# Kernel tuning notes

Measured on AMD Instinct MI355X. Metric: run time of the kernel, lower is better.

Reference implementation:

```python
import jax, jax.numpy as jnp
import numpy as np
from jax.ops import segment_sum, segment_max

N, E, B = 100000, 400000, 2048
F_NODE, F_EDGE, G_DIM = 7, 3, 10
HID, H, C, L, T = 128, 4, 32, 4, 5
EPS = 1e-5
NEG_SLOPE = 0.2

def setup_inputs():
    key = jax.random.key(0)
    ks = iter(jax.random.split(key, 64))
    def nrm(shape, fan_in):
        return jax.random.normal(next(ks), shape, jnp.float32) / np.float32(np.sqrt(fan_in))
    return {
        "x": jax.random.normal(next(ks), (N, F_NODE), jnp.float32),
        "edge_index": jax.random.randint(next(ks), (2, E), 0, N),
        "edge_attr": jax.random.normal(next(ks), (E, F_EDGE), jnp.float32),
        "batch": jnp.sort(jax.random.randint(next(ks), (N,), 0, B)),
        "global_features": jax.random.normal(next(ks), (B, G_DIM), jnp.float32),
        "node_w": nrm((F_NODE, HID), F_NODE), "node_b": jnp.zeros((HID,), jnp.float32),
        "edge_w": nrm((F_EDGE, HID), F_EDGE), "edge_b": jnp.zeros((HID,), jnp.float32),
        "gat_lin_w": nrm((L, HID, H * C), HID),
        "gat_edge_w": nrm((L, HID, H * C), HID),
        "att_src": nrm((L, H, C), C), "att_dst": nrm((L, H, C), C), "att_edge": nrm((L, H, C), C),
        "gat_bias": jnp.zeros((L, H * C), jnp.float32),
        "bn_gamma": jnp.ones((L, HID), jnp.float32), "bn_beta": jnp.zeros((L, HID), jnp.float32),
        "bn_mean": jnp.zeros((L, HID), jnp.float32), "bn_var": jnp.ones((L, HID), jnp.float32),
        "gc_w": nrm((3 * HID, HID), 3 * HID), "gc_b": jnp.zeros((HID,), jnp.float32),
        "gf1_w": nrm((G_DIM, HID // 2), G_DIM), "gf1_b": jnp.zeros((HID // 2,), jnp.float32),
        "gf2_w": nrm((HID // 2, HID // 2), HID // 2), "gf2_b": jnp.zeros((HID // 2,), jnp.float32),
        "p1_w": nrm((HID + HID // 2, HID), HID + HID // 2), "p1_b": jnp.zeros((HID,), jnp.float32),
        "p2_w": nrm((HID, HID // 2), HID), "p2_b": jnp.zeros((HID // 2,), jnp.float32),
        "p3_w": nrm((HID // 2, T), HID // 2), "p3_b": jnp.zeros((T,), jnp.float32),
    }

def _forward(x, edge_attr, global_features,
             node_w, node_b, edge_w, edge_b,
             gat_lin_w, gat_edge_w, att_src, att_dst, att_edge, gat_bias,
             bn_gamma, bn_beta, bn_mean, bn_var,
             gc_w, gc_b, gf1_w, gf1_b, gf2_w, gf2_b,
             p1_w, p1_b, p2_w, p2_b, p3_w, p3_b,
             edge_index, batch):
    n = x.shape[0]
    b = global_features.shape[0]
    src, dst = edge_index[0], edge_index[1]
    loop = jnp.arange(n)

    h = x @ node_w + node_b                       # [N, HID]
    e = edge_attr @ edge_w + edge_b               # [E, HID]

    # PyG add_self_loops with fill_value='mean': self-loop edge feature is the
    # mean of incoming edge features (0 for isolated nodes).
    deg = segment_sum(jnp.ones((src.shape[0],), h.dtype), dst, num_segments=n)
    e_loop = segment_sum(e, dst, num_segments=n) / jnp.maximum(deg, 1.0)[:, None]
    fsrc = jnp.concatenate([src, loop])
    fdst = jnp.concatenate([dst, loop])
    fe = jnp.concatenate([e, e_loop], axis=0)     # [E+N, HID]

    for i in range(L):
        h_res = h
        xh = (h @ gat_lin_w[i]).reshape(n, H, C)
        eh = (fe @ gat_edge_w[i]).reshape(-1, H, C)
        a_s = jnp.einsum('nhc,hc->nh', xh, att_src[i])
        a_d = jnp.einsum('nhc,hc->nh', xh, att_dst[i])
        a_e = jnp.einsum('ehc,hc->eh', eh, att_edge[i])
        alpha = jax.nn.leaky_relu(a_s[fsrc] + a_d[fdst] + a_e, NEG_SLOPE)  # [E+N, H]
        # segment softmax over destination neighborhoods (self loops => nonempty)
        amax = segment_max(alpha, fdst, num_segments=n)
        expa = jnp.exp(alpha - amax[fdst])
        denom = segment_sum(expa, fdst, num_segments=n)
        coef = expa / denom[fdst]
        out = segment_sum(xh[fsrc] * coef[..., None], fdst, num_segments=n)
        out = out.reshape(n, H * C) + gat_bias[i]
        # BatchNorm (eval-mode running stats)
        out = (out - bn_mean[i]) * (bn_gamma[i] / jnp.sqrt(bn_var[i] + EPS)) + bn_beta[i]
        h = jax.nn.relu(out) + h_res

    # multi-pool readout
    cnt = segment_sum(jnp.ones((n,), h.dtype), batch, num_segments=b)
    gsum = segment_sum(h, batch, num_segments=b)
    gmean = gsum / jnp.maximum(cnt, 1.0)[:, None]
    gmax = segment_max(h, batch, num_segments=b)
    gmax = jnp.where(cnt[:, None] > 0, gmax, 0.0)
    graph = jnp.concatenate([gmean, gmax, gsum], axis=1)   # [B, 3*HID]
    graph = jax.nn.relu(graph @ gc_w + gc_b)
    glob = jax.nn.relu(global_features @ gf1_w + gf1_b) @ gf2_w + gf2_b
    comb = jnp.concatenate([graph, glob], axis=1)          # [B, HID + HID//2]
    hid = jax.nn.relu(comb @ p1_w + p1_b)
    hid = jax.nn.relu(hid @ p2_w + p2_b)
    return hid @ p3_w + p3_b                               # [B, T]

def reference(x, edge_index, edge_attr, batch, global_features,
              node_w, node_b, edge_w, edge_b,
              gat_lin_w, gat_edge_w, att_src, att_dst, att_edge, gat_bias,
              bn_gamma, bn_beta, bn_mean, bn_var,
              gc_w, gc_b, gf1_w, gf1_b, gf2_w, gf2_b,
              p1_w, p1_b, p2_w, p2_b, p3_w, p3_b):
    return _forward(x, edge_attr, global_features,
                    node_w, node_b, edge_w, edge_b,
                    gat_lin_w, gat_edge_w, att_src, att_dst, att_edge, gat_bias,
                    bn_gamma, bn_beta, bn_mean, bn_var,
                    gc_w, gc_b, gf1_w, gf1_b, gf2_w, gf2_b,
                    p1_w, p1_b, p2_w, p2_b, p3_w, p3_b,
                    edge_index, batch)
```

## Files before the change

kernel.cpp:

```cpp
#include <hip/hip_runtime.h>

#define N_NODES 100000
#define N_EDGES 400000
#define N_GRAPHS 2048
#define HID 128
#define NLAYER 4
#define TOUT 5
#define EPSV 1e-5f
#define SLOPE 0.2f
#define MAXDEG 32
#define NB 98

typedef float v4f __attribute__((ext_vector_type(4)));
typedef __bf16 v8bf __attribute__((ext_vector_type(8)));

static __device__ __forceinline__ unsigned short f2bf_bits(float f){
  unsigned u = __builtin_bit_cast(unsigned, f);
  unsigned r = u + 0x7fffu + ((u >> 16) & 1u);
  return (unsigned short)(r >> 16);
}
static __device__ __forceinline__ float bfbits2f(unsigned short s){
  unsigned u = ((unsigned)s) << 16;
  return __builtin_bit_cast(float, u);
}
static __device__ __forceinline__ float bflo(unsigned u){
  return __builtin_bit_cast(float, u << 16);
}
static __device__ __forceinline__ float bfhi(unsigned u){
  return __builtin_bit_cast(float, u & 0xffff0000u);
}
static __device__ __forceinline__ float lrelu(float v){
  return v>0.f ? v : SLOPE*v;
}


__global__ void k_setup(const float* __restrict__ gat_edge_w, const float* __restrict__ att_edge,
                        const float* __restrict__ edge_w, const float* __restrict__ edge_b,
                        const float* __restrict__ gat_bias, const float* __restrict__ gamma,
                        const float* __restrict__ beta, const float* __restrict__ mean,
                        const float* __restrict__ var, const float* __restrict__ gat_lin_w,
                        const float* __restrict__ att_src, const float* __restrict__ att_dst,
                        float* __restrict__ mebuf, float* __restrict__ bnA, float* __restrict__ bnS,
                        unsigned short* __restrict__ whiE, unsigned short* __restrict__ wloE,
                        unsigned short* __restrict__ whi,
                        int* __restrict__ deg, int* __restrict__ fill){
  __shared__ float Ve[128*16];
  int bid = blockIdx.x, t = threadIdx.x;
  if(bid == 0){
    for(int i=t; i<NLAYER*HID; i+=256){
      int l_ = i>>7, pos = i&127, lane = pos>>2, j = pos&3;
      int ch = ((lane>>3)<<5) + ((lane&7)<<1) + ((j&1)<<4) + (j>>1);
      int src = l_*128 + ch;
      float A = gamma[src]*rsqrtf(var[src]+EPSV);
      bnA[i] = A;
      bnS[i] = (gat_bias[src]-mean[src])*A + beta[src];
    }
    for(int id=t; id<2048; id+=256){
      int k = id>>4, li = id&15, l = li>>2, hh = li&3;
      const float* gw = gat_edge_w + l*16384 + k*128 + hh*32;
      const float* at = att_edge + l*128 + hh*32;
      float s = 0.f;
      #pragma unroll
      for(int c=0;c<32;++c) s += gw[c]*at[c];
      Ve[k*16+li] = s;
    }
    __syncthreads();
    if(t < 48){
      int f = t>>4, li = t&15;
      float s=0.f;
      for(int k=0;k<128;++k) s += edge_w[f*128+k]*Ve[k*16+li];
      mebuf[f*16+li] = s;
    } else if (t < 64){
      int li = t-48; float s=0.f;
      for(int k=0;k<128;++k) s += edge_b[k]*Ve[k*16+li];
      mebuf[48+li] = s;
    }
  } else if(bid <= 1024){
    int wave = t>>6, lane = t&63;
    int i = (bid-1)*8 + wave*2 + (lane>>5);
    int l_ = i>>11, rest = i&2047, kp = rest>>4, col = rest&15;
    int sub = lane&31;
    float val = 0.f;
    if(col < 8){
      int h_ = col&3, isdst = col>>2;
      int ch = ((kp>>5)<<5) + ((kp&1)<<4) + ((kp&31)>>1);
      const float* at = (isdst? att_dst : att_src);
      val = gat_lin_w[l_*16384 + ch*128 + h_*32 + sub] * at[l_*128 + h_*32 + sub];
    }
    val += __shfl_xor(val,1); val += __shfl_xor(val,2); val += __shfl_xor(val,4);
    val += __shfl_xor(val,8); val += __shfl_xor(val,16);
    if(sub == 0){
      unsigned short hi = f2bf_bits(val);
      unsigned short lo = f2bf_bits(val - bfbits2f(hi));
      int kb=kp>>5, quad=(kp>>3)&3, jj=kp&7, lane2=quad*16+col;
      int dst = ((l_*4+kb)*64 + lane2)*8 + jj;
      whiE[dst]=hi; wloE[dst]=lo;
    }
  } else if(bid <= 1280){
    int tg = (bid-1025)*256 + t;
    int base = tg>>9, off = tg&511;
    int l = base>>5, kb=(base>>3)&3, cg=base&7;
    int lane = off>>3, j = off&7;
    int quad = lane>>4, r = lane&15;
    int kp = kb*32 + quad*8 + j;
    int k = ((kp>>5)<<5) | ((kp&1)<<4) | ((kp&31)>>1);
    whi[tg] = f2bf_bits(gat_lin_w[l*16384 + k*128 + cg*16 + r]);
  } else {
    int tg = (bid-1281)*256 + t;
    if(tg < N_NODES){ deg[tg]=0; fill[tg]=0; }
  }
}

__global__ void k_init(const float* __restrict__ x, const float* __restrict__ nw,
                       const float* __restrict__ nb, unsigned* __restrict__ h16,
                       const int* __restrict__ ei, int* __restrict__ deg){
  int bid = blockIdx.x, t = threadIdx.x;
  if(bid < N_NODES/4){
    int node = bid*4 + (t>>6);
    int c = t&63;
    int ch = ((c>>4)<<5) + (c&15);
    float a0 = nb[ch], a1 = nb[ch+16];
    #pragma unroll
    for(int f=0; f<7; ++f){
      float xv = x[node*7+f];
      a0 += xv*nw[f*HID+ch];
      a1 += xv*nw[f*HID+ch+16];
    }
    unsigned p = (unsigned)f2bf_bits(a0) | ((unsigned)f2bf_bits(a1)<<16);
    h16[(size_t)node*64 + c] = p;
  } else {
    int e = (bid - N_NODES/4)*256 + t;
    if(e < N_EDGES) atomicAdd(&deg[ei[N_EDGES+e]], 1);
  }
}

__global__ void k_scan1(const int* __restrict__ deg, int* __restrict__ part){
  __shared__ int s[256];
  int t=threadIdx.x; int base = blockIdx.x*1024 + t*4;
  int sum=0;
  #pragma unroll
  for(int j=0;j<4;++j){ int i=base+j; sum += (i<N_NODES)? deg[i]:0; }
  s[t]=sum; __syncthreads();
  for(int off=128; off>0; off>>=1){ if(t<off) s[t]+=s[t+off]; __syncthreads(); }
  if(t==0) part[blockIdx.x]=s[0];
}
__global__ void k_scan3(const int* __restrict__ deg, const int* __restrict__ part,
                        int* __restrict__ rowptr){
  __shared__ int s[256];
  int t=threadIdx.x, b=blockIdx.x;
  int g = 0, tot = 0;
  for(int i=0;i<NB;++i){ int v = part[i]; g += (i<b)? v : 0; tot += v; }
  if(b==0 && t==0) rowptr[N_NODES]=tot;
  int base = b*1024 + t*4;
  int v[4]; int sum=0; int pre[4];
  #pragma unroll
  for(int j=0;j<4;++j){ int i=base+j; v[j]=(i<N_NODES)?deg[i]:0; pre[j]=sum; sum+=v[j]; }
  s[t]=sum; __syncthreads();
  for(int off=1; off<256; off<<=1){
    int xv = (t>=off)? s[t-off]:0; __syncthreads();
    s[t]+=xv; __syncthreads();
  }
  int toff = (t>0)? s[t-1]:0;
  #pragma unroll
  for(int j=0;j<4;++j){ int i=base+j; if(i<N_NODES) rowptr[i]=g+toff+pre[j]; }
}

__global__ void k_fill(const int* __restrict__ ei, const float* __restrict__ ea,
                       const int* __restrict__ rowptr, int* __restrict__ fill,
                       int* __restrict__ csr_src, float* __restrict__ ea_csr){
  int e = blockIdx.x*256+threadIdx.x;
  if(e>=N_EDGES) return;
  int dst = ei[N_EDGES+e];
  int pos = rowptr[dst] + atomicAdd(&fill[dst],1);
  csr_src[pos] = ei[e];
  v4f q = {ea[e*3], ea[e*3+1], ea[e*3+2], 0.f};
  ((v4f*)ea_csr)[pos] = q;
}

__global__ void k_gemm(const unsigned short* __restrict__ h16,
                       const unsigned short* __restrict__ whi,
                       const unsigned short* __restrict__ whiE,
                       const unsigned short* __restrict__ wloE,
                       unsigned* __restrict__ xhb, float* __restrict__ as_, float* __restrict__ ad_){
  __shared__ unsigned sxh[4][2][16*68];
  int wave = threadIdx.x>>6, lane = threadIdx.x&63;
  int base = blockIdx.x*128;
  int q = lane>>4, r = lane&15;
  int r0[2];
  r0[0] = base + wave*16;
  r0[1] = base + 64 + wave*16;
  if(r0[0] > N_NODES-16) r0[0] = N_NODES-16;
  if(r0[1] > N_NODES-16) r0[1] = N_NODES-16;
  v8bf av[2][4];
  #pragma unroll
  for(int tt=0;tt<2;++tt){
    const unsigned short* hrow = h16 + (size_t)(r0[tt] + r)*HID;
    #pragma unroll
    for(int kb=0;kb<4;++kb)
      av[tt][kb] = *(const v8bf*)(hrow + kb*32 + q*8);
  }
  v4f acc[2][8];
  #pragma unroll
  for(int cg=0;cg<8;++cg){
    v4f a0 = {0.f,0.f,0.f,0.f}, a1 = {0.f,0.f,0.f,0.f};
    #pragma unroll
    for(int kb=0;kb<4;++kb){
      v8bf bhi = *(const v8bf*)(whi + ((kb*8+cg)*64 + lane)*8);
      a0 = __builtin_amdgcn_mfma_f32_16x16x32_bf16(av[0][kb], bhi, a0, 0,0,0);
      a1 = __builtin_amdgcn_mfma_f32_16x16x32_bf16(av[1][kb], bhi, a1, 0,0,0);
    }
    acc[0][cg]=a0; acc[1][cg]=a1;
  }
  v4f acc8[2] = {{0.f,0.f,0.f,0.f},{0.f,0.f,0.f,0.f}};
  #pragma unroll
  for(int kb=0;kb<4;++kb){
    v8bf bhi = *(const v8bf*)(whiE + (kb*64 + lane)*8);
    v8bf blo = *(const v8bf*)(wloE + (kb*64 + lane)*8);
    #pragma unroll
    for(int tt=0;tt<2;++tt){
      acc8[tt] = __builtin_amdgcn_mfma_f32_16x16x32_bf16(av[tt][kb], blo, acc8[tt], 0,0,0);
      acc8[tt] = __builtin_amdgcn_mfma_f32_16x16x32_bf16(av[tt][kb], bhi, acc8[tt], 0,0,0);
    }
  }
  #pragma unroll
  for(int tt=0;tt<2;++tt){
    #pragma unroll
    for(int m=0;m<4;++m){
      #pragma unroll
      for(int reg=0;reg<4;++reg){
        unsigned pack = (unsigned)f2bf_bits(acc[tt][2*m][reg]) | ((unsigned)f2bf_bits(acc[tt][2*m+1][reg])<<16);
        sxh[wave][tt][(q*4+reg)*68 + m*16 + r] = pack;
      }
    }
  }
  __syncthreads();
  {
    int rr = lane>>4, c4 = lane&15;
    #pragma unroll
    for(int tt=0;tt<2;++tt){
      #pragma unroll
      for(int rg=0; rg<4; ++rg){
        int i = rg*4 + rr;
        uint4 v = *(const uint4*)&sxh[wave][tt][i*68 + c4*4];
        *(uint4*)(xhb + (size_t)(r0[tt] + i)*64 + c4*4) = v;
      }
    }
  }
  #pragma unroll
  for(int tt=0;tt<2;++tt){
    if(r < 4){
      #pragma unroll
      for(int reg=0;reg<4;++reg)
        as_[(size_t)(r0[tt] + q*4 + reg)*4 + r] = acc8[tt][reg];
    } else if(r < 8){
      #pragma unroll
      for(int reg=0;reg<4;++reg)
        ad_[(size_t)(r0[tt] + q*4 + reg)*4 + (r-4)] = acc8[tt][reg];
    }
  }
}

__global__ void k_aggr(const unsigned* __restrict__ xhb, const float* __restrict__ as_,
    const float* __restrict__ ad_, const float* __restrict__ ea_csr,
    const float* __restrict__ mebuf,
    const int* __restrict__ rowptr, const int* __restrict__ csr_src,
    const float* __restrict__ bnA_l, const float* __restrict__ bnS_l,
    unsigned* __restrict__ h16, int layer){
  __shared__ float lds_coef[4][MAXDEG*4];
  __shared__ int   lds_src[4][MAXDEG];
  int w = threadIdx.x>>6, lane = threadIdx.x&63;
  int node = blockIdx.x*4 + w;
  if(node >= N_NODES) return;
  int s = rowptr[node], e = rowptr[node+1];
  int deg = e - s;
  int l = lane&31, half = lane>>5, hh2 = l>>3;
  const uint2* xrow = (const uint2*)xhb;
  float a0,a1,a2,a3;

  if(deg <= MAXDEG){
    int eidx = lane>>2, h = lane&3;
    int li = layer*4+h;
    float mec0=mebuf[li], mec1=mebuf[16+li], mec2=mebuf[32+li], meb=mebuf[48+li];
    float ad_h = ad_[node*4+h];
    int j0 = eidx;
    float t0 = 0.f, g0 = 0.f;
    int s0 = node;
    bool v0 = (j0 < deg);
    if(v0){
      s0 = csr_src[s+j0];
      v4f qq = ((const v4f*)ea_csr)[s+j0];
      t0 = qq.x*mec0 + qq.y*mec1 + qq.z*mec2;
      g0 = lrelu(as_[s0*4+h] + ad_h + t0 + meb);
    }
    float ts, ds, inv;
    if(deg <= 16){
      ts = t0;
      ts += __shfl_xor(ts,4); ts += __shfl_xor(ts,8);
      ts += __shfl_xor(ts,16); ts += __shfl_xor(ts,32);
      float lt = (deg>0) ? ts/(float)deg + meb : 0.f;
      float al = lrelu(as_[node*4+h] + ad_h + lt);
      float e0 = v0 ? __expf(g0-al) : 0.f;
      ds = e0;
      ds += __shfl_xor(ds,4); ds += __shfl_xor(ds,8);
      ds += __shfl_xor(ds,16); ds += __shfl_xor(ds,32);
      inv = 1.f/(ds+1.f);
      lds_src[w][j0] = s0;
      lds_coef[w][j0*4+h] = e0*inv;
    } else {
      int j1 = 16+eidx;
      float t1 = 0.f, g1 = 0.f;
      int s1 = node;
      bool v1 = (j1 < deg);
      if(v1){
        s1 = csr_src[s+j1];
        v4f qq = ((const v4f*)ea_csr)[s+j1];
        t1 = qq.x*mec0 + qq.y*mec1 + qq.z*mec2;
        g1 = lrelu(as_[s1*4+h] + ad_h + t1 + meb);
      }
      ts = t0+t1;
      ts += __shfl_xor(ts,4); ts += __shfl_xor(ts,8);
      ts += __shfl_xor(ts,16); ts += __shfl_xor(ts,32);
      float lt = ts/(float)deg + meb;
      float al = lrelu(as_[node*4+h] + ad_h + lt);
      float e0 = v0 ? __expf(g0-al) : 0.f;
      float e1 = v1 ? __expf(g1-al) : 0.f;
      ds = e0+e1;
      ds += __shfl_xor(ds,4); ds += __shfl_xor(ds,8);
      ds += __shfl_xor(ds,16); ds += __shfl_xor(ds,32);
      inv = 1.f/(ds+1.f);
      if(h==0){ lds_src[w][j0]=s0; lds_src[w][j1]=s1; }
      lds_coef[w][j0*4+h] = e0*inv;
      lds_coef[w][j1*4+h] = e1*inv;
    }
    float cs4 = __shfl(inv, hh2);
    uint2 su = xrow[(size_t)node*32 + l];
    int pdeg = (deg+3)&~3;
    a0=a1=a2=a3=0.f;
    for(int j=0;j<pdeg;j+=4){
      float ca = lds_coef[w][(j+half)*4+hh2];
      float cb = lds_coef[w][(j+2+half)*4+hh2];
      int sa = lds_src[w][j+half], sb = lds_src[w][j+2+half];
      uint2 ua = xrow[(size_t)sa*32+l];
      uint2 ub = xrow[(size_t)sb*32+l];
      a0 += ca*bflo(ua.x) + cb*bflo(ub.x);
      a1 += ca*bfhi(ua.x) + cb*bfhi(ub.x);
      a2 += ca*bflo(ua.y) + cb*bflo(ub.y);
      a3 += ca*bfhi(ua.y) + cb*bfhi(ub.y);
    }
    a0 += __shfl_xor(a0,32); a1 += __shfl_xor(a1,32);
    a2 += __shfl_xor(a2,32); a3 += __shfl_xor(a3,32);
    a0 += cs4*bflo(su.x); a1 += cs4*bfhi(su.x);
    a2 += cs4*bflo(su.y); a3 += cs4*bfhi(su.y);
  } else {
    int li = layer*4+hh2;
    float mec0=mebuf[li], mec1=mebuf[16+li], mec2=mebuf[32+li], meb=mebuf[48+li];
    float adv = ad_[node*4+hh2];
    float ts = 0.f;
    for(int j=s;j<e;++j){
      v4f qq = ((const v4f*)ea_csr)[j];
      ts += qq.x*mec0 + qq.y*mec1 + qq.z*mec2;
    }
    float al = lrelu(as_[node*4+hh2] + adv + ts/(float)deg + meb);
    float m = al, d = 1.f;
    uint2 su = xrow[(size_t)node*32 + l];
    float c0=bflo(su.x),c1=bfhi(su.x),c2=bflo(su.y),c3=bfhi(su.y);
    for(int j=s;j<e;++j){
      int sr = csr_src[j];
      v4f qq = ((const v4f*)ea_csr)[j];
      float b = lrelu(as_[sr*4+hh2] + adv + qq.x*mec0+qq.y*mec1+qq.z*mec2+meb);
      uint2 uv = xrow[(size_t)sr*32 + l];
      float nm = fmaxf(m,b);
      float sc = __expf(m-nm), eb = __expf(b-nm);
      d = d*sc + eb;
      c0 = c0*sc + eb*bflo(uv.x); c1 = c1*sc + eb*bfhi(uv.x);
      c2 = c2*sc + eb*bflo(uv.y); c3 = c3*sc + eb*bfhi(uv.y);
      m = nm;
    }
    float inv2 = 1.f/d;
    a0=c0*inv2; a1=c1*inv2; a2=c2*inv2; a3=c3*inv2;
  }

  if(half==0){
    const v4f* A4 = (const v4f*)bnA_l;
    const v4f* S4 = (const v4f*)bnS_l;
    v4f A = A4[l], S = S4[l];
    uint2 hr = ((const uint2*)h16)[(size_t)node*32 + l];
    float o0 = fmaxf(a0*A.x+S.x, 0.f) + bflo(hr.x);
    float o1 = fmaxf(a1*A.y+S.y, 0.f) + bfhi(hr.x);
    float o2 = fmaxf(a2*A.z+S.z, 0.f) + bflo(hr.y);
    float o3 = fmaxf(a3*A.w+S.w, 0.f) + bfhi(hr.y);
    uint2 p;
    p.x = (unsigned)f2bf_bits(o0) | ((unsigned)f2bf_bits(o1)<<16);
    p.y = (unsigned)f2bf_bits(o2) | ((unsigned)f2bf_bits(o3)<<16);
    ((uint2*)h16)[(size_t)node*32 + l] = p;
  }
}

__global__ void k_tail(const unsigned* __restrict__ h16, const int* __restrict__ batch,
   const float* __restrict__ gf,
   const float* __restrict__ gc_w, const float* __restrict__ gc_b,
   const float* __restrict__ gf1_w, const float* __restrict__ gf1_b,
   const float* __restrict__ gf2_w, const float* __restrict__ gf2_b,
   const float* __restrict__ p1_w, const float* __restrict__ p1_b,
   const float* __restrict__ p2_w, const float* __restrict__ p2_b,
   const float* __restrict__ p3_w, const float* __restrict__ p3_b,
   float* __restrict__ out){
  __shared__ float sg[384];
  __shared__ int sb[2];
  __shared__ float comb[192];
  __shared__ float hid1[64];
  __shared__ float r1[128];
  __shared__ float r2[64];
  int g = blockIdx.x, t = threadIdx.x;
  if(t < 2){
    int target = g + t;
    int lo=0, hi=N_NODES;
    while(lo<hi){ int mid=(lo+hi)>>1; if(batch[mid] < target) lo=mid+1; else hi=mid; }
    sb[t]=lo;
  }
  __syncthreads();
  {
    int s = sb[0], e = sb[1];
    int u = ((t>>5)<<4) + (t&15);
    int hiflag = (t>>4)&1;
    float sum=0.f, mx=-3.4e38f;
    for(int i=s;i<e;++i){
      unsigned uv = h16[(size_t)i*64 + u];
      float v = hiflag ? bfhi(uv) : bflo(uv);
      sum+=v; mx=fmaxf(mx,v);
    }
    int cnt = e-s;
    float meanv = sum / (float)(cnt>1?cnt:1);
    if(cnt==0) mx=0.f;
    sg[t] = meanv;
    sg[128+t] = mx;
    sg[256+t] = sum;
  }
  if(t<64){
    float a = gf1_b[t];
    #pragma unroll
    for(int i=0;i<10;++i) a += gf[g*10+i]*gf1_w[i*64+t];
    hid1[t] = fmaxf(a,0.f);
  }
  __syncthreads();
  if(t<64){
    float a = gf2_b[t];
    for(int k=0;k<64;++k) a += hid1[k]*gf2_w[k*64+t];
    comb[128+t] = a;
  }
  {
    float a = gc_b[t];
    for(int k=0;k<384;++k) a += sg[k]*gc_w[k*128+t];
    comb[t] = fmaxf(a,0.f);
  }
  __syncthreads();
  {
    float a = p1_b[t];
    for(int k=0;k<192;++k) a += comb[k]*p1_w[k*128+t];
    r1[t] = fmaxf(a,0.f);
  }
  __syncthreads();
  if(t<64){
    float a = p2_b[t];
    for(int k=0;k<128;++k) a += r1[k]*p2_w[k*64+t];
    r2[t] = fmaxf(a,0.f);
  }
  __syncthreads();
  if(t<TOUT){
    float a = p3_b[t];
    for(int k=0;k<64;++k) a += r2[k]*p3_w[k*TOUT+t];
    out[g*TOUT+t] = a;
  }
}

extern "C" void kernel_launch(void* const* d_in, const int* in_sizes, int n_in,
                              void* d_out, int out_size, void* d_ws, size_t ws_size,
                              hipStream_t stream){
  (void)in_sizes; (void)n_in; (void)out_size; (void)ws_size;
  const float* x        = (const float*)d_in[0];
  const int*   ei       = (const int*)d_in[1];
  const float* ea       = (const float*)d_in[2];
  const int*   batch    = (const int*)d_in[3];
  const float* gfin     = (const float*)d_in[4];
  const float* node_w   = (const float*)d_in[5];
  const float* node_b   = (const float*)d_in[6];
  const float* edge_w   = (const float*)d_in[7];
  const float* edge_b   = (const float*)d_in[8];
  const float* gat_lin_w  = (const float*)d_in[9];
  const float* gat_edge_w = (const float*)d_in[10];
  const float* att_src  = (const float*)d_in[11];
  const float* att_dst  = (const float*)d_in[12];
  const float* att_edge = (const float*)d_in[13];
  const float* gat_bias = (const float*)d_in[14];
  const float* bn_gamma = (const float*)d_in[15];
  const float* bn_beta  = (const float*)d_in[16];
  const float* bn_mean  = (const float*)d_in[17];
  const float* bn_var   = (const float*)d_in[18];
  const float* gc_w = (const float*)d_in[19];
  const float* gc_b = (const float*)d_in[20];
  const float* gf1_w = (const float*)d_in[21];
  const float* gf1_b = (const float*)d_in[22];
  const float* gf2_w = (const float*)d_in[23];
  const float* gf2_b = (const float*)d_in[24];
  const float* p1_w = (const float*)d_in[25];
  const float* p1_b = (const float*)d_in[26];
  const float* p2_w = (const float*)d_in[27];
  const float* p2_b = (const float*)d_in[28];
  const float* p3_w = (const float*)d_in[29];
  const float* p3_b = (const float*)d_in[30];
  float* out = (float*)d_out;

  char* w = (char*)d_ws;
  size_t o = 0;
  auto carve = [&](size_t bytes)->char*{
    char* p = w + o; o += (bytes + 255) & ~(size_t)255; return p;
  };
  unsigned* xhb = (unsigned*)carve((size_t)N_NODES*64*4);
  unsigned* h16 = (unsigned*)carve((size_t)N_NODES*64*4);
  float* ea_csr = (float*)carve((size_t)N_EDGES*4*4);
  float* as_    = (float*)carve((size_t)N_NODES*4*4);
  float* ad_    = (float*)carve((size_t)N_NODES*4*4);
  int* deg      = (int*)carve((size_t)N_NODES*4);
  int* rowptr   = (int*)carve((size_t)(N_NODES+1)*4);
  int* fill     = (int*)carve((size_t)N_NODES*4);
  int* csr_src  = (int*)carve((size_t)N_EDGES*4);
  int* part     = (int*)carve(1024*4);
  float* mebuf  = (float*)carve(64*4);
  float* bnA    = (float*)carve((size_t)NLAYER*HID*4);
  float* bnS    = (float*)carve((size_t)NLAYER*HID*4);
  unsigned short* whi = (unsigned short*)carve(65536*2);
  unsigned short* whiE = (unsigned short*)carve(8192*2);
  unsigned short* wloE = (unsigned short*)carve(8192*2);

  int zb = (N_NODES+255)/256;
  k_setup<<<1 + 1024 + 256 + zb, 256, 0, stream>>>(gat_edge_w, att_edge, edge_w, edge_b,
        gat_bias, bn_gamma, bn_beta, bn_mean, bn_var,
        gat_lin_w, att_src, att_dst, mebuf, bnA, bnS, whiE, wloE, whi, deg, fill);
  k_init<<<N_NODES/4 + (N_EDGES+255)/256, 256, 0, stream>>>(x, node_w, node_b, h16, ei, deg);
  k_scan1<<<NB,256,0,stream>>>(deg, part);
  k_scan3<<<NB,256,0,stream>>>(deg, part, rowptr);
  k_fill<<<(N_EDGES+255)/256,256,0,stream>>>(ei, ea, rowptr, fill, csr_src, ea_csr);

  for(int l=0;l<NLAYER;++l){
    k_gemm<<<(N_NODES+127)/128,256,0,stream>>>((const unsigned short*)h16,
        whi + l*16384, whiE + l*2048, wloE + l*2048,
        xhb, as_, ad_);
    k_aggr<<<(N_NODES+3)/4,256,0,stream>>>(xhb, as_, ad_, ea_csr, mebuf,
        rowptr, csr_src, bnA + l*128, bnS + l*128, h16, l);
  }

  k_tail<<<N_GRAPHS,128,0,stream>>>(h16, batch, gfin, gc_w, gc_b, gf1_w, gf1_b,
        gf2_w, gf2_b, p1_w, p1_b, p2_w, p2_b, p3_w, p3_b, out);
}
```

Measured before the change: 520.8 us.

## Restructure setup kernels: parallelize edge-attention precompute, fuse CSR fill into first GEMM

The edge-attention vector precompute, which ran serially in a single block, is spread across 16 blocks using wave shuffles. Node embedding init moves into the setup kernel, degree counting becomes its own small kernel, and the CSR fill runs as extra blocks of the layer-0 GEMM launch. The aim is fewer serialized launches and a shorter critical path in setup. The trade-off is extra code branching, and the GEMM kernel now carries the fill's parameters.

```diff
diff --git a/kernel.cpp b/kernel.cpp
--- a/kernel.cpp
+++ b/kernel.cpp
@@ -10,6 +10,7 @@
 #define SLOPE 0.2f
 #define MAXDEG 32
 #define NB 98
+#define GEMM_BLOCKS 782
 
 typedef float v4f __attribute__((ext_vector_type(4)));
 typedef __bf16 v8bf __attribute__((ext_vector_type(8)));
@@ -40,13 +41,33 @@
                         const float* __restrict__ beta, const float* __restrict__ mean,
                         const float* __restrict__ var, const float* __restrict__ gat_lin_w,
                         const float* __restrict__ att_src, const float* __restrict__ att_dst,
+                        const float* __restrict__ x, const float* __restrict__ nw,
+                        const float* __restrict__ nb, unsigned* __restrict__ h16,
                         float* __restrict__ mebuf, float* __restrict__ bnA, float* __restrict__ bnS,
                         unsigned short* __restrict__ whiE, unsigned short* __restrict__ wloE,
                         unsigned short* __restrict__ whi,
                         int* __restrict__ deg, int* __restrict__ fill){
-  __shared__ float Ve[128*16];
   int bid = blockIdx.x, t = threadIdx.x;
-  if(bid == 0){
+  if(bid < 16){
+    int wv = t>>6, lane = t&63;
+    int o = bid*4 + wv;
+    int li = (o<48)? (o&15) : (o-48);
+    int f = o>>4;
+    int l = li>>2, hh = li&3;
+    int c = lane&31, kk = lane>>5;
+    float at_c = att_edge[l*128 + hh*32 + c];
+    float acc = 0.f;
+    #pragma unroll 8
+    for(int t2=0; t2<64; ++t2){
+      int k = kk*64 + t2;
+      float wk = (o<48)? edge_w[f*128+k] : edge_b[k];
+      acc += wk * gat_edge_w[l*16384 + k*128 + hh*32 + c];
+    }
+    acc *= at_c;
+    acc += __shfl_xor(acc,1); acc += __shfl_xor(acc,2); acc += __shfl_xor(acc,4);
+    acc += __shfl_xor(acc,8); acc += __shfl_xor(acc,16); acc += __shfl_xor(acc,32);
+    if(lane==0) mebuf[o] = acc;
+  } else if(bid == 16){
     for(int i=t; i<NLAYER*HID; i+=256){
       int l_ = i>>7, pos = i&127, lane = pos>>2, j = pos&3;
       int ch = ((lane>>3)<<5) + ((lane&7)<<1) + ((j&1)<<4) + (j>>1);
@@ -55,29 +76,9 @@
       bnA[i] = A;
       bnS[i] = (gat_bias[src]-mean[src])*A + beta[src];
     }
-    for(int id=t; id<2048; id+=256){
-      int k = id>>4, li = id&15, l = li>>2, hh = li&3;
-      const float* gw = gat_edge_w + l*16384 + k*128 + hh*32;
-      const float* at = att_edge + l*128 + hh*32;
-      float s = 0.f;
-      #pragma unroll
-      for(int c=0;c<32;++c) s += gw[c]*at[c];
-      Ve[k*16+li] = s;
-    }
-    __syncthreads();
-    if(t < 48){
-      int f = t>>4, li = t&15;
-      float s=0.f;
-      for(int k=0;k<128;++k) s += edge_w[f*128+k]*Ve[k*16+li];
-      mebuf[f*16+li] = s;
-    } else if (t < 64){
-      int li = t-48; float s=0.f;
-      for(int k=0;k<128;++k) s += edge_b[k]*Ve[k*16+li];
-      mebuf[48+li] = s;
-    }
-  } else if(bid <= 1024){
+  } else if(bid <= 1040){
     int wave = t>>6, lane = t&63;
-    int i = (bid-1)*8 + wave*2 + (lane>>5);
+    int i = (bid-17)*8 + wave*2 + (lane>>5);
     int l_ = i>>11, rest = i&2047, kp = rest>>4, col = rest&15;
     int sub = lane&31;
     float val = 0.f;
@@ -96,8 +97,8 @@
       int dst = ((l_*4+kb)*64 + lane2)*8 + jj;
       whiE[dst]=hi; wloE[dst]=lo;
     }
-  } else if(bid <= 1280){
-    int tg = (bid-1025)*256 + t;
+  } else if(bid <= 1296){
+    int tg = (bid-1041)*256 + t;
     int base = tg>>9, off = tg&511;
     int l = base>>5, kb=(base>>3)&3, cg=base&7;
     int lane = off>>3, j = off&7;
@@ -105,18 +106,11 @@
     int kp = kb*32 + quad*8 + j;
     int k = ((kp>>5)<<5) | ((kp&1)<<4) | ((kp&31)>>1);
     whi[tg] = f2bf_bits(gat_lin_w[l*16384 + k*128 + cg*16 + r]);
+  } else if(bid <= 1687){
+    int tg = (bid-1297)*256 + t;
+    if(tg < N_NODES){ deg[tg]=0; fill[tg]=0; }
   } else {
-    int tg = (bid-1281)*256 + t;
-    if(tg < N_NODES){ deg[tg]=0; fill[tg]=0; }
-  }
-}
-
-__global__ void k_init(const float* __restrict__ x, const float* __restrict__ nw,
-                       const float* __restrict__ nb, unsigned* __restrict__ h16,
-                       const int* __restrict__ ei, int* __restrict__ deg){
-  int bid = blockIdx.x, t = threadIdx.x;
-  if(bid < N_NODES/4){
-    int node = bid*4 + (t>>6);
+    int node = (bid-1688)*4 + (t>>6);
     int c = t&63;
     int ch = ((c>>4)<<5) + (c&15);
     float a0 = nb[ch], a1 = nb[ch+16];
@@ -128,10 +122,12 @@
     }
     unsigned p = (unsigned)f2bf_bits(a0) | ((unsigned)f2bf_bits(a1)<<16);
     h16[(size_t)node*64 + c] = p;
-  } else {
-    int e = (bid - N_NODES/4)*256 + t;
-    if(e < N_EDGES) atomicAdd(&deg[ei[N_EDGES+e]], 1);
-  }
+  }
+}
+
+__global__ void k_deg(const int* __restrict__ ei, int* __restrict__ deg){
+  int e = blockIdx.x*256 + threadIdx.x;
+  if(e < N_EDGES) atomicAdd(&deg[ei[N_EDGES+e]], 1);
 }
 
 __global__ void k_scan1(const int* __restrict__ deg, int* __restrict__ part){
@@ -165,23 +161,25 @@
   for(int j=0;j<4;++j){ int i=base+j; if(i<N_NODES) rowptr[i]=g+toff+pre[j]; }
 }
 
-__global__ void k_fill(const int* __restrict__ ei, const float* __restrict__ ea,
-                       const int* __restrict__ rowptr, int* __restrict__ fill,
-                       int* __restrict__ csr_src, float* __restrict__ ea_csr){
-  int e = blockIdx.x*256+threadIdx.x;
-  if(e>=N_EDGES) return;
-  int dst = ei[N_EDGES+e];
-  int pos = rowptr[dst] + atomicAdd(&fill[dst],1);
-  csr_src[pos] = ei[e];
-  v4f q = {ea[e*3], ea[e*3+1], ea[e*3+2], 0.f};
-  ((v4f*)ea_csr)[pos] = q;
-}
-
 __global__ void k_gemm(const unsigned short* __restrict__ h16,
                        const unsigned short* __restrict__ whi,
                        const unsigned short* __restrict__ whiE,
                        const unsigned short* __restrict__ wloE,
-                       unsigned* __restrict__ xhb, float* __restrict__ as_, float* __restrict__ ad_){
+                       unsigned* __restrict__ xhb, float* __restrict__ as_, float* __restrict__ ad_,
+                       const int* __restrict__ ei, const float* __restrict__ ea,
+                       const int* __restrict__ rowptr, int* __restrict__ fill,
+                       int* __restrict__ csr_src, float* __restrict__ ea_csr){
+  if(blockIdx.x >= GEMM_BLOCKS){
+    int e = (blockIdx.x - GEMM_BLOCKS)*256 + threadIdx.x;
+    if(e < N_EDGES){
+      int dst = ei[N_EDGES+e];
+      int pos = rowptr[dst] + atomicAdd(&fill[dst],1);
+      csr_src[pos] = ei[e];
+      v4f q = {ea[e*3], ea[e*3+1], ea[e*3+2], 0.f};
+      ((v4f*)ea_csr)[pos] = q;
+    }
+    return;
+  }
   __shared__ unsigned sxh[4][2][16*68];
   int wave = threadIdx.x>>6, lane = threadIdx.x&63;
   int base = blockIdx.x*128;
@@ -532,19 +530,19 @@
   unsigned short* whiE = (unsigned short*)carve(8192*2);
   unsigned short* wloE = (unsigned short*)carve(8192*2);
 
-  int zb = (N_NODES+255)/256;
-  k_setup<<<1 + 1024 + 256 + zb, 256, 0, stream>>>(gat_edge_w, att_edge, edge_w, edge_b,
+  k_setup<<<1688 + N_NODES/4, 256, 0, stream>>>(gat_edge_w, att_edge, edge_w, edge_b,
         gat_bias, bn_gamma, bn_beta, bn_mean, bn_var,
-        gat_lin_w, att_src, att_dst, mebuf, bnA, bnS, whiE, wloE, whi, deg, fill);
-  k_init<<<N_NODES/4 + (N_EDGES+255)/256, 256, 0, stream>>>(x, node_w, node_b, h16, ei, deg);
+        gat_lin_w, att_src, att_dst, x, node_w, node_b, h16,
+        mebuf, bnA, bnS, whiE, wloE, whi, deg, fill);
+  k_deg<<<(N_EDGES+255)/256, 256, 0, stream>>>(ei, deg);
   k_scan1<<<NB,256,0,stream>>>(deg, part);
   k_scan3<<<NB,256,0,stream>>>(deg, part, rowptr);
-  k_fill<<<(N_EDGES+255)/256,256,0,stream>>>(ei, ea, rowptr, fill, csr_src, ea_csr);
 
   for(int l=0;l<NLAYER;++l){
-    k_gemm<<<(N_NODES+127)/128,256,0,stream>>>((const unsigned short*)h16,
+    int gb = (l==0) ? GEMM_BLOCKS + (N_EDGES+255)/256 : GEMM_BLOCKS;
+    k_gemm<<<gb,256,0,stream>>>((const unsigned short*)h16,
         whi + l*16384, whiE + l*2048, wloE + l*2048,
-        xhb, as_, ad_);
+        xhb, as_, ad_, ei, ea, rowptr, fill, csr_src, ea_csr);
     k_aggr<<<(N_NODES+3)/4,256,0,stream>>>(xhb, as_, ad_, ea_csr, mebuf,
         rowptr, csr_src, bnA + l*128, bnS + l*128, h16, l);
   }
```

After: 495.0 us. -5.0%, faster.
